# Kernel tuning notes

Measured on AMD Instinct MI355X. Metric: run time of the kernel, lower is better.

## Reference

```python
import jax, jax.numpy as jnp
import numpy as np

N_NODES = 100000
N_EDGES = 50000
NNZ = 800000
D_IN = 128
D_OUT = 128


def setup_inputs() -> dict:
    key = jax.random.key(0)
    k1, k2, k3, k4, k5 = jax.random.split(key, 5)
    x_0 = jax.random.normal(k1, (N_NODES, D_IN), dtype=jnp.float32)
    W = jax.random.normal(k2, (D_OUT, D_IN), dtype=jnp.float32) / np.sqrt(D_IN)
    b = jax.random.normal(k3, (D_OUT,), dtype=jnp.float32) * 0.01
    node_ids = jax.random.randint(k4, (NNZ,), 0, N_NODES, dtype=jnp.int32)
    edge_ids = jax.random.randint(k5, (NNZ,), 0, N_EDGES, dtype=jnp.int32)
    return {"x_0": x_0, "W": W, "b": b, "node_ids": node_ids, "edge_ids": edge_ids}


def reference(x_0, W, b, node_ids, edge_ids):
    # Linear transform (no batchnorm: use_bn=False)
    x = x_0 @ W.T + b  # [n_nodes, out_channels]

    # Step 1: hyperedge aggregation (e_aggr='sum'):  m_{0->1} = B_1^T x, reduce=sum
    m01 = jax.ops.segment_sum(x[node_ids], edge_ids, num_segments=N_EDGES)  # [n_edges, d]

    # Step 2: node aggregation (v_aggr='mean'):  m_{1->0} = B_1 m_{0->1}, reduce=mean
    s = jax.ops.segment_sum(m01[edge_ids], node_ids, num_segments=N_NODES)  # [n_nodes, d]
    cnt = jax.ops.segment_sum(jnp.ones((NNZ,), dtype=x.dtype), node_ids, num_segments=N_NODES)
    m10 = s / jnp.maximum(cnt, 1.0)[:, None]

    # Step 3: SAGE update (residual add)
    return x + m10
```

## Files before the change

kernel.cpp:

```cpp
#include <hip/hip_runtime.h>
#include <hip/hip_bf16.h>

#define NN 100000
#define NE 50000
#define NZ 800000
#define D  128
#define NSEG (NE + NN)
#define FILL_P 4
#define FILL_B 782
#define G_GEMM 782
#define G_HIST 391

typedef __bf16 bf16x8 __attribute__((ext_vector_type(8)));
typedef float f32x4 __attribute__((ext_vector_type(4)));

static __device__ __forceinline__ unsigned short f2bf(float f) {
  union { float f; unsigned u; } v; v.f = f;
  unsigned r = (v.u + 0x7FFFu + ((v.u >> 16) & 1u)) >> 16;
  return (unsigned short)r;
}
static __device__ __forceinline__ float bf2f(unsigned short h) {
  union { unsigned u; float f; } v; v.u = ((unsigned)h) << 16;
  return v.f;
}

__global__ __launch_bounds__(256) void unisage_gemm_hist(const float* __restrict__ x0,
                                                         const float* __restrict__ W,
                                                         const float* __restrict__ bias,
                                                         unsigned short* __restrict__ xb,
                                                         const int* __restrict__ nid,
                                                         const int* __restrict__ eid,
                                                         int* __restrict__ cnt,
                                                         unsigned int* __restrict__ rank) {
  __shared__ __bf16 Wl[128][136];
  if (blockIdx.x < G_GEMM) {
    const int t = threadIdx.x;
#pragma unroll
    for (int i = 0; i < 16; ++i) {
      int idx = i * 1024 + t * 4;
      int dout = idx >> 7;
      int k = idx & 127;
      float4 wv = *(const float4*)(W + idx);
      Wl[dout][k + 0] = (__bf16)wv.x;
      Wl[dout][k + 1] = (__bf16)wv.y;
      Wl[dout][k + 2] = (__bf16)wv.z;
      Wl[dout][k + 3] = (__bf16)wv.w;
    }
    __syncthreads();

    const int wave = t >> 6;
    const int lane = t & 63;
    const int lr = lane & 15;
    const int lg = lane >> 4;
    const int rowbase = blockIdx.x * 128 + wave * 32;

    f32x4 acc[2][8] = {};

#pragma unroll
    for (int ks = 0; ks < 4; ++ks) {
      const int k0 = ks * 32 + lg * 8;
      bf16x8 b[8];
#pragma unroll
      for (int cf = 0; cf < 8; ++cf)
        b[cf] = *(const bf16x8*)&Wl[cf * 16 + lr][k0];
#pragma unroll
      for (int rf = 0; rf < 2; ++rf) {
        int row = rowbase + rf * 16 + lr;
        row = row < NN ? row : NN - 1;
        const float* src = x0 + (size_t)row * D + k0;
        float4 f0 = *(const float4*)(src);
        float4 f1 = *(const float4*)(src + 4);
        bf16x8 a;
        a[0] = (__bf16)f0.x; a[1] = (__bf16)f0.y;
        a[2] = (__bf16)f0.z; a[3] = (__bf16)f0.w;
        a[4] = (__bf16)f1.x; a[5] = (__bf16)f1.y;
        a[6] = (__bf16)f1.z; a[7] = (__bf16)f1.w;
#pragma unroll
        for (int cf = 0; cf < 8; ++cf)
          acc[rf][cf] = __builtin_amdgcn_mfma_f32_16x16x32_bf16(a, b[cf], acc[rf][cf], 0, 0, 0);
      }
    }

#pragma unroll
    for (int cf = 0; cf < 8; ++cf) {
      float bv = bias[cf * 16 + lr];
#pragma unroll
      for (int rf = 0; rf < 2; ++rf) {
#pragma unroll
        for (int r = 0; r < 4; ++r) {
          int row = rowbase + rf * 16 + lg * 4 + r;
          if (row < NN)
            xb[(size_t)row * D + cf * 16 + lr] = f2bf(acc[rf][cf][r] + bv);
        }
      }
    }
  } else {
    int base = ((blockIdx.x - G_GEMM) * 256 + threadIdx.x) * 8;
    if (base >= NZ) return;
    int4 ea = *(const int4*)(eid + base);
    int4 eb = *(const int4*)(eid + base + 4);
    int4 na = *(const int4*)(nid + base);
    int4 nb = *(const int4*)(nid + base + 4);
    int e[8] = {ea.x, ea.y, ea.z, ea.w, eb.x, eb.y, eb.z, eb.w};
    int v[8] = {na.x, na.y, na.z, na.w, nb.x, nb.y, nb.z, nb.w};
    unsigned re[8], rn[8];
#pragma unroll
    for (int j = 0; j < 8; ++j) re[j] = (unsigned)atomicAdd(&cnt[e[j]], 1);
#pragma unroll
    for (int j = 0; j < 8; ++j) rn[j] = (unsigned)atomicAdd(&cnt[NE + v[j]], 1);
    uint4 r0, r1;
    r0.x = (re[0] & 0xffffu) | (rn[0] << 16);
    r0.y = (re[1] & 0xffffu) | (rn[1] << 16);
    r0.z = (re[2] & 0xffffu) | (rn[2] << 16);
    r0.w = (re[3] & 0xffffu) | (rn[3] << 16);
    r1.x = (re[4] & 0xffffu) | (rn[4] << 16);
    r1.y = (re[5] & 0xffffu) | (rn[5] << 16);
    r1.z = (re[6] & 0xffffu) | (rn[6] << 16);
    r1.w = (re[7] & 0xffffu) | (rn[7] << 16);
    *(uint4*)(rank + base) = r0;
    *(uint4*)(rank + base + 4) = r1;
  }
}

__global__ void unisage_scan_k1(const int* __restrict__ in, int* __restrict__ bsum, int n) {
  __shared__ int sh[256];
  int t = threadIdx.x;
  int base = blockIdx.x * 1024 + t * 4;
  int s = 0;
#pragma unroll
  for (int j = 0; j < 4; ++j)
    if (base + j < n) s += in[base + j];
  sh[t] = s;
  __syncthreads();
  for (int o = 128; o > 0; o >>= 1) {
    if (t < o) sh[t] += sh[t + o];
    __syncthreads();
  }
  if (t == 0) bsum[blockIdx.x] = sh[0];
}

__global__ void unisage_scan_k3(const int* __restrict__ in, const int* __restrict__ bsum,
                                int* __restrict__ out, int n, int nb) {
  __shared__ int sh[256];
  int t = threadIdx.x;
  int bv = (t < nb) ? bsum[t] : 0;
  sh[t] = bv;
  __syncthreads();
  for (int o = 1; o < 256; o <<= 1) {
    int add = (t >= o) ? sh[t - o] : 0;
    __syncthreads();
    sh[t] += add;
    __syncthreads();
  }
  int bbase = (blockIdx.x == 0) ? 0 : sh[blockIdx.x - 1];
  __syncthreads();

  int base = blockIdx.x * 1024 + t * 4;
  int v[4];
#pragma unroll
  for (int j = 0; j < 4; ++j) v[j] = (base + j < n) ? in[base + j] : 0;
  int tsum = v[0] + v[1] + v[2] + v[3];
  sh[t] = tsum;
  __syncthreads();
  for (int o = 1; o < 256; o <<= 1) {
    int add = (t >= o) ? sh[t - o] : 0;
    __syncthreads();
    sh[t] += add;
    __syncthreads();
  }
  int run = sh[t] - tsum + bbase;
#pragma unroll
  for (int j = 0; j < 4; ++j) {
    if (base + j < n) out[base + j] = run;
    run += v[j];
  }
}

__global__ void unisage_fill(const int* __restrict__ nid, const int* __restrict__ eid,
                             const unsigned int* __restrict__ rank,
                             const int* __restrict__ off,
                             int* __restrict__ csr_e, int* __restrict__ csr_n) {
  const int R = (NSEG + FILL_P - 1) / FILL_P;
  int pass = blockIdx.x / FILL_B;
  int base = ((blockIdx.x % FILL_B) * 256 + threadIdx.x) * 4;
  if (base >= NZ) return;
  int lo = pass * R, hi = lo + R;
  int4 e4 = *(const int4*)(eid + base);
  int4 n4 = *(const int4*)(nid + base);
  uint4 r4 = *(const uint4*)(rank + base);
  int e[4] = {e4.x, e4.y, e4.z, e4.w};
  int v[4] = {n4.x, n4.y, n4.z, n4.w};
  unsigned r[4] = {r4.x, r4.y, r4.z, r4.w};
#pragma unroll
  for (int j = 0; j < 4; ++j) {
    if (e[j] >= lo && e[j] < hi) csr_e[off[e[j]] + (int)(r[j] & 0xffffu)] = v[j];
    int s = NE + v[j];
    if (s >= lo && s < hi) csr_n[off[s] + (int)(r[j] >> 16) - NZ] = e[j];
  }
}

#define QRED(x) { x += __shfl_xor(x, 16, 64); x += __shfl_xor(x, 32, 64); }

__global__ void unisage_edge_agg(const unsigned short* __restrict__ xb,
                                 const int* __restrict__ csr_e,
                                 const int* __restrict__ off, const int* __restrict__ cnt,
                                 unsigned short* __restrict__ m01b) {
  int w = (blockIdx.x * 256 + threadIdx.x) >> 6;
  int lane = threadIdx.x & 63;
  if (w >= NE) return;
  int quad = lane >> 4;
  int sl = lane & 15;
  int beg = off[w];
  int deg = cnt[w];
  int end = beg + deg;
  float a0 = 0, a1 = 0, a2 = 0, a3 = 0, a4 = 0, a5 = 0, a6 = 0, a7 = 0;
  for (int base = beg; base < end; base += 64) {
    int m = min(64, end - base);
    int idx = (lane < m) ? csr_e[base + lane] : 0;
    int iters = (m + 3) >> 2;
    for (int jj = 0; jj < iters; ++jj) {
      int p = 4 * jj + quad;
      int r = __shfl(idx, p, 64);
      if (p < m) {
        uint4 vv = *(const uint4*)(xb + (size_t)r * D + sl * 8);
        a0 += bf2f((unsigned short)(vv.x & 0xffffu)); a1 += bf2f((unsigned short)(vv.x >> 16));
        a2 += bf2f((unsigned short)(vv.y & 0xffffu)); a3 += bf2f((unsigned short)(vv.y >> 16));
        a4 += bf2f((unsigned short)(vv.z & 0xffffu)); a5 += bf2f((unsigned short)(vv.z >> 16));
        a6 += bf2f((unsigned short)(vv.w & 0xffffu)); a7 += bf2f((unsigned short)(vv.w >> 16));
      }
    }
  }
  QRED(a0) QRED(a1) QRED(a2) QRED(a3) QRED(a4) QRED(a5) QRED(a6) QRED(a7)
  if (quad == 0) {
    uint4 o;
    o.x = (unsigned)f2bf(a0) | ((unsigned)f2bf(a1) << 16);
    o.y = (unsigned)f2bf(a2) | ((unsigned)f2bf(a3) << 16);
    o.z = (unsigned)f2bf(a4) | ((unsigned)f2bf(a5) << 16);
    o.w = (unsigned)f2bf(a6) | ((unsigned)f2bf(a7) << 16);
    *(uint4*)(m01b + (size_t)w * D + sl * 8) = o;
  }
}

__global__ void unisage_node_agg(const unsigned short* __restrict__ xb,
                                 const unsigned short* __restrict__ m01b,
                                 const int* __restrict__ csr_n,
                                 const int* __restrict__ off, const int* __restrict__ cnt,
                                 float* __restrict__ out) {
  int w = (blockIdx.x * 256 + threadIdx.x) >> 6;
  int lane = threadIdx.x & 63;
  if (w >= NN) return;
  int quad = lane >> 4;
  int sl = lane & 15;
  int deg = cnt[NE + w];
  int beg = off[NE + w] - NZ;
  int end = beg + deg;
  float a0 = 0, a1 = 0, a2 = 0, a3 = 0, a4 = 0, a5 = 0, a6 = 0, a7 = 0;
  for (int base = beg; base < end; base += 64) {
    int m = min(64, end - base);
    int idx = (lane < m) ? csr_n[base + lane] : 0;
    int iters = (m + 3) >> 2;
    for (int jj = 0; jj < iters; ++jj) {
      int p = 4 * jj + quad;
      int r = __shfl(idx, p, 64);
      if (p < m) {
        uint4 vv = *(const uint4*)(m01b + (size_t)r * D + sl * 8);
        a0 += bf2f((unsigned short)(vv.x & 0xffffu)); a1 += bf2f((unsigned short)(vv.x >> 16));
        a2 += bf2f((unsigned short)(vv.y & 0xffffu)); a3 += bf2f((unsigned short)(vv.y >> 16));
        a4 += bf2f((unsigned short)(vv.z & 0xffffu)); a5 += bf2f((unsigned short)(vv.z >> 16));
        a6 += bf2f((unsigned short)(vv.w & 0xffffu)); a7 += bf2f((unsigned short)(vv.w >> 16));
      }
    }
  }
  QRED(a0) QRED(a1) QRED(a2) QRED(a3) QRED(a4) QRED(a5) QRED(a6) QRED(a7)
  if (quad == 0) {
    float inv = 1.0f / fmaxf((float)deg, 1.0f);
    uint4 xr = *(const uint4*)(xb + (size_t)w * D + sl * 8);
    float4 o0, o1;
    o0.x = bf2f((unsigned short)(xr.x & 0xffffu)) + a0 * inv;
    o0.y = bf2f((unsigned short)(xr.x >> 16))     + a1 * inv;
    o0.z = bf2f((unsigned short)(xr.y & 0xffffu)) + a2 * inv;
    o0.w = bf2f((unsigned short)(xr.y >> 16))     + a3 * inv;
    o1.x = bf2f((unsigned short)(xr.z & 0xffffu)) + a4 * inv;
    o1.y = bf2f((unsigned short)(xr.z >> 16))     + a5 * inv;
    o1.z = bf2f((unsigned short)(xr.w & 0xffffu)) + a6 * inv;
    o1.w = bf2f((unsigned short)(xr.w >> 16))     + a7 * inv;
    *(float4*)(out + (size_t)w * D + sl * 8) = o0;
    *(float4*)(out + (size_t)w * D + sl * 8 + 4) = o1;
  }
}

extern "C" void kernel_launch(void* const* d_in, const int* in_sizes, int n_in,
                              void* d_out, int out_size, void* d_ws, size_t ws_size,
                              hipStream_t stream) {
  const float* x0   = (const float*)d_in[0];
  const float* W    = (const float*)d_in[1];
  const float* bias = (const float*)d_in[2];
  const int* nid    = (const int*)d_in[3];
  const int* eid    = (const int*)d_in[4];
  float* out = (float*)d_out;

  unsigned short* xb   = (unsigned short*)d_ws;
  unsigned short* m01b = xb + (size_t)NN * D;
  int* cnt   = (int*)(m01b + (size_t)NE * D);
  int* off   = cnt + 150016;
  unsigned int* rank = (unsigned int*)(off + 150016);
  int* csr_e = (int*)(rank + NZ);
  int* csr_n = csr_e + NZ;
  int* bsum  = csr_n + NZ;

  hipMemsetAsync(cnt, 0, NSEG * sizeof(int), stream);

  unisage_gemm_hist<<<G_GEMM + G_HIST, 256, 0, stream>>>(x0, W, bias, xb, nid, eid, cnt, rank);

  const int nb = (NSEG + 1023) / 1024;
  unisage_scan_k1<<<nb, 256, 0, stream>>>(cnt, bsum, NSEG);
  unisage_scan_k3<<<nb, 256, 0, stream>>>(cnt, bsum, off, NSEG, nb);

  unisage_fill<<<FILL_P * FILL_B, 256, 0, stream>>>(nid, eid, rank, off, csr_e, csr_n);

  unisage_edge_agg<<<(NE * 64) / 256, 256, 0, stream>>>(xb, csr_e, off, cnt, m01b);
  unisage_node_agg<<<(NN * 64) / 256, 256, 0, stream>>>(xb, m01b, csr_n, off, cnt, out);
}
```

Measured before the change: 211.1 us.

## Split fused GEMM/histogram kernel, unroll gather loops by two, halve fill passes

The combined GEMM+histogram launch is split back into two separate kernels, giving up the overlap of the atomic histogram with the MFMA GEMM in exchange for simpler per-kernel occupancy. The edge and node gather loops are unrolled by two with predicated (multiply-by-zero) accumulation so two row loads can be in flight at once. The CSR fill pass count is halved from 4 to 2. Together these trade fusion-based overlap for more memory-level parallelism in the gathers and fewer fill passes.

```diff
diff --git a/kernel.cpp b/kernel.cpp
--- a/kernel.cpp
+++ b/kernel.cpp
@@ -6,10 +6,8 @@
 #define NZ 800000
 #define D  128
 #define NSEG (NE + NN)
-#define FILL_P 4
+#define FILL_P 2
 #define FILL_B 782
-#define G_GEMM 782
-#define G_HIST 391
 
 typedef __bf16 bf16x8 __attribute__((ext_vector_type(8)));
 typedef float f32x4 __attribute__((ext_vector_type(4)));
@@ -24,102 +22,99 @@
   return v.f;
 }
 
-__global__ __launch_bounds__(256) void unisage_gemm_hist(const float* __restrict__ x0,
+__global__ __launch_bounds__(256) void unisage_gemm_mfma(const float* __restrict__ x0,
                                                          const float* __restrict__ W,
                                                          const float* __restrict__ bias,
-                                                         unsigned short* __restrict__ xb,
-                                                         const int* __restrict__ nid,
-                                                         const int* __restrict__ eid,
-                                                         int* __restrict__ cnt,
-                                                         unsigned int* __restrict__ rank) {
+                                                         unsigned short* __restrict__ xb) {
   __shared__ __bf16 Wl[128][136];
-  if (blockIdx.x < G_GEMM) {
-    const int t = threadIdx.x;
-#pragma unroll
-    for (int i = 0; i < 16; ++i) {
-      int idx = i * 1024 + t * 4;
-      int dout = idx >> 7;
-      int k = idx & 127;
-      float4 wv = *(const float4*)(W + idx);
-      Wl[dout][k + 0] = (__bf16)wv.x;
-      Wl[dout][k + 1] = (__bf16)wv.y;
-      Wl[dout][k + 2] = (__bf16)wv.z;
-      Wl[dout][k + 3] = (__bf16)wv.w;
-    }
-    __syncthreads();
-
-    const int wave = t >> 6;
-    const int lane = t & 63;
-    const int lr = lane & 15;
-    const int lg = lane >> 4;
-    const int rowbase = blockIdx.x * 128 + wave * 32;
-
-    f32x4 acc[2][8] = {};
-
-#pragma unroll
-    for (int ks = 0; ks < 4; ++ks) {
-      const int k0 = ks * 32 + lg * 8;
-      bf16x8 b[8];
+  const int t = threadIdx.x;
+#pragma unroll
+  for (int i = 0; i < 16; ++i) {
+    int idx = i * 1024 + t * 4;
+    int dout = idx >> 7;
+    int k = idx & 127;
+    float4 wv = *(const float4*)(W + idx);
+    Wl[dout][k + 0] = (__bf16)wv.x;
+    Wl[dout][k + 1] = (__bf16)wv.y;
+    Wl[dout][k + 2] = (__bf16)wv.z;
+    Wl[dout][k + 3] = (__bf16)wv.w;
+  }
+  __syncthreads();
+
+  const int wave = t >> 6;
+  const int lane = t & 63;
+  const int lr = lane & 15;
+  const int lg = lane >> 4;
+  const int rowbase = blockIdx.x * 128 + wave * 32;
+
+  f32x4 acc[2][8] = {};
+
+#pragma unroll
+  for (int ks = 0; ks < 4; ++ks) {
+    const int k0 = ks * 32 + lg * 8;
+    bf16x8 b[8];
+#pragma unroll
+    for (int cf = 0; cf < 8; ++cf)
+      b[cf] = *(const bf16x8*)&Wl[cf * 16 + lr][k0];
+#pragma unroll
+    for (int rf = 0; rf < 2; ++rf) {
+      int row = rowbase + rf * 16 + lr;
+      row = row < NN ? row : NN - 1;
+      const float* src = x0 + (size_t)row * D + k0;
+      float4 f0 = *(const float4*)(src);
+      float4 f1 = *(const float4*)(src + 4);
+      bf16x8 a;
+      a[0] = (__bf16)f0.x; a[1] = (__bf16)f0.y;
+      a[2] = (__bf16)f0.z; a[3] = (__bf16)f0.w;
+      a[4] = (__bf16)f1.x; a[5] = (__bf16)f1.y;
+      a[6] = (__bf16)f1.z; a[7] = (__bf16)f1.w;
 #pragma unroll
       for (int cf = 0; cf < 8; ++cf)
-        b[cf] = *(const bf16x8*)&Wl[cf * 16 + lr][k0];
-#pragma unroll
-      for (int rf = 0; rf < 2; ++rf) {
-        int row = rowbase + rf * 16 + lr;
-        row = row < NN ? row : NN - 1;
-        const float* src = x0 + (size_t)row * D + k0;
-        float4 f0 = *(const float4*)(src);
-        float4 f1 = *(const float4*)(src + 4);
-        bf16x8 a;
-        a[0] = (__bf16)f0.x; a[1] = (__bf16)f0.y;
-        a[2] = (__bf16)f0.z; a[3] = (__bf16)f0.w;
-        a[4] = (__bf16)f1.x; a[5] = (__bf16)f1.y;
-        a[6] = (__bf16)f1.z; a[7] = (__bf16)f1.w;
-#pragma unroll
-        for (int cf = 0; cf < 8; ++cf)
-          acc[rf][cf] = __builtin_amdgcn_mfma_f32_16x16x32_bf16(a, b[cf], acc[rf][cf], 0, 0, 0);
+        acc[rf][cf] = __builtin_amdgcn_mfma_f32_16x16x32_bf16(a, b[cf], acc[rf][cf], 0, 0, 0);
+    }
+  }
+
+#pragma unroll
+  for (int cf = 0; cf < 8; ++cf) {
+    float bv = bias[cf * 16 + lr];
+#pragma unroll
+    for (int rf = 0; rf < 2; ++rf) {
+#pragma unroll
+      for (int r = 0; r < 4; ++r) {
+        int row = rowbase + rf * 16 + lg * 4 + r;
+        if (row < NN)
+          xb[(size_t)row * D + cf * 16 + lr] = f2bf(acc[rf][cf][r] + bv);
       }
     }
-
-#pragma unroll
-    for (int cf = 0; cf < 8; ++cf) {
-      float bv = bias[cf * 16 + lr];
-#pragma unroll
-      for (int rf = 0; rf < 2; ++rf) {
-#pragma unroll
-        for (int r = 0; r < 4; ++r) {
-          int row = rowbase + rf * 16 + lg * 4 + r;
-          if (row < NN)
-            xb[(size_t)row * D + cf * 16 + lr] = f2bf(acc[rf][cf][r] + bv);
-        }
-      }
-    }
-  } else {
-    int base = ((blockIdx.x - G_GEMM) * 256 + threadIdx.x) * 8;
-    if (base >= NZ) return;
-    int4 ea = *(const int4*)(eid + base);
-    int4 eb = *(const int4*)(eid + base + 4);
-    int4 na = *(const int4*)(nid + base);
-    int4 nb = *(const int4*)(nid + base + 4);
-    int e[8] = {ea.x, ea.y, ea.z, ea.w, eb.x, eb.y, eb.z, eb.w};
-    int v[8] = {na.x, na.y, na.z, na.w, nb.x, nb.y, nb.z, nb.w};
-    unsigned re[8], rn[8];
-#pragma unroll
-    for (int j = 0; j < 8; ++j) re[j] = (unsigned)atomicAdd(&cnt[e[j]], 1);
-#pragma unroll
-    for (int j = 0; j < 8; ++j) rn[j] = (unsigned)atomicAdd(&cnt[NE + v[j]], 1);
-    uint4 r0, r1;
-    r0.x = (re[0] & 0xffffu) | (rn[0] << 16);
-    r0.y = (re[1] & 0xffffu) | (rn[1] << 16);
-    r0.z = (re[2] & 0xffffu) | (rn[2] << 16);
-    r0.w = (re[3] & 0xffffu) | (rn[3] << 16);
-    r1.x = (re[4] & 0xffffu) | (rn[4] << 16);
-    r1.y = (re[5] & 0xffffu) | (rn[5] << 16);
-    r1.z = (re[6] & 0xffffu) | (rn[6] << 16);
-    r1.w = (re[7] & 0xffffu) | (rn[7] << 16);
-    *(uint4*)(rank + base) = r0;
-    *(uint4*)(rank + base + 4) = r1;
-  }
+  }
+}
+
+__global__ void unisage_hist_rank(const int* __restrict__ nid, const int* __restrict__ eid,
+                                  int* __restrict__ cnt, unsigned int* __restrict__ rank) {
+  int base = (blockIdx.x * 256 + threadIdx.x) * 8;
+  if (base >= NZ) return;
+  int4 ea = *(const int4*)(eid + base);
+  int4 eb = *(const int4*)(eid + base + 4);
+  int4 na = *(const int4*)(nid + base);
+  int4 nb = *(const int4*)(nid + base + 4);
+  int e[8] = {ea.x, ea.y, ea.z, ea.w, eb.x, eb.y, eb.z, eb.w};
+  int v[8] = {na.x, na.y, na.z, na.w, nb.x, nb.y, nb.z, nb.w};
+  unsigned re[8], rn[8];
+#pragma unroll
+  for (int j = 0; j < 8; ++j) re[j] = (unsigned)atomicAdd(&cnt[e[j]], 1);
+#pragma unroll
+  for (int j = 0; j < 8; ++j) rn[j] = (unsigned)atomicAdd(&cnt[NE + v[j]], 1);
+  uint4 r0, r1;
+  r0.x = (re[0] & 0xffffu) | (rn[0] << 16);
+  r0.y = (re[1] & 0xffffu) | (rn[1] << 16);
+  r0.z = (re[2] & 0xffffu) | (rn[2] << 16);
+  r0.w = (re[3] & 0xffffu) | (rn[3] << 16);
+  r1.x = (re[4] & 0xffffu) | (rn[4] << 16);
+  r1.y = (re[5] & 0xffffu) | (rn[5] << 16);
+  r1.z = (re[6] & 0xffffu) | (rn[6] << 16);
+  r1.w = (re[7] & 0xffffu) | (rn[7] << 16);
+  *(uint4*)(rank + base) = r0;
+  *(uint4*)(rank + base + 4) = r1;
 }
 
 __global__ void unisage_scan_k1(const int* __restrict__ in, int* __restrict__ bsum, int n) {
@@ -201,6 +196,20 @@
 
 #define QRED(x) { x += __shfl_xor(x, 16, 64); x += __shfl_xor(x, 32, 64); }
 
+__device__ __forceinline__ void acc_row(const unsigned short* __restrict__ tab,
+                                        int row, int sl, bool valid, float* a) {
+  uint4 vv = *(const uint4*)(tab + (size_t)row * D + sl * 8);
+  float w = valid ? 1.f : 0.f;
+  a[0] += w * bf2f((unsigned short)(vv.x & 0xffffu));
+  a[1] += w * bf2f((unsigned short)(vv.x >> 16));
+  a[2] += w * bf2f((unsigned short)(vv.y & 0xffffu));
+  a[3] += w * bf2f((unsigned short)(vv.y >> 16));
+  a[4] += w * bf2f((unsigned short)(vv.z & 0xffffu));
+  a[5] += w * bf2f((unsigned short)(vv.z >> 16));
+  a[6] += w * bf2f((unsigned short)(vv.w & 0xffffu));
+  a[7] += w * bf2f((unsigned short)(vv.w >> 16));
+}
+
 __global__ void unisage_edge_agg(const unsigned short* __restrict__ xb,
                                  const int* __restrict__ csr_e,
                                  const int* __restrict__ off, const int* __restrict__ cnt,
@@ -213,30 +222,33 @@
   int beg = off[w];
   int deg = cnt[w];
   int end = beg + deg;
-  float a0 = 0, a1 = 0, a2 = 0, a3 = 0, a4 = 0, a5 = 0, a6 = 0, a7 = 0;
+  float a[8] = {};
   for (int base = beg; base < end; base += 64) {
     int m = min(64, end - base);
     int idx = (lane < m) ? csr_e[base + lane] : 0;
     int iters = (m + 3) >> 2;
-    for (int jj = 0; jj < iters; ++jj) {
-      int p = 4 * jj + quad;
-      int r = __shfl(idx, p, 64);
-      if (p < m) {
-        uint4 vv = *(const uint4*)(xb + (size_t)r * D + sl * 8);
-        a0 += bf2f((unsigned short)(vv.x & 0xffffu)); a1 += bf2f((unsigned short)(vv.x >> 16));
-        a2 += bf2f((unsigned short)(vv.y & 0xffffu)); a3 += bf2f((unsigned short)(vv.y >> 16));
-        a4 += bf2f((unsigned short)(vv.z & 0xffffu)); a5 += bf2f((unsigned short)(vv.z >> 16));
-        a6 += bf2f((unsigned short)(vv.w & 0xffffu)); a7 += bf2f((unsigned short)(vv.w >> 16));
-      }
-    }
-  }
-  QRED(a0) QRED(a1) QRED(a2) QRED(a3) QRED(a4) QRED(a5) QRED(a6) QRED(a7)
+    int jj = 0;
+    for (; jj + 1 < iters; jj += 2) {
+      int p0 = 4 * jj + quad;
+      int p1 = p0 + 4;
+      int r0 = __shfl(idx, p0, 64);
+      int r1 = __shfl(idx, p1, 64);
+      acc_row(xb, r0, sl, p0 < m, a);
+      acc_row(xb, r1, sl, p1 < m, a);
+    }
+    if (jj < iters) {
+      int p0 = 4 * jj + quad;
+      int r0 = __shfl(idx, p0, 64);
+      acc_row(xb, r0, sl, p0 < m, a);
+    }
+  }
+  QRED(a[0]) QRED(a[1]) QRED(a[2]) QRED(a[3]) QRED(a[4]) QRED(a[5]) QRED(a[6]) QRED(a[7])
   if (quad == 0) {
     uint4 o;
-    o.x = (unsigned)f2bf(a0) | ((unsigned)f2bf(a1) << 16);
-    o.y = (unsigned)f2bf(a2) | ((unsigned)f2bf(a3) << 16);
-    o.z = (unsigned)f2bf(a4) | ((unsigned)f2bf(a5) << 16);
-    o.w = (unsigned)f2bf(a6) | ((unsigned)f2bf(a7) << 16);
+    o.x = (unsigned)f2bf(a[0]) | ((unsigned)f2bf(a[1]) << 16);
+    o.y = (unsigned)f2bf(a[2]) | ((unsigned)f2bf(a[3]) << 16);
+    o.z = (unsigned)f2bf(a[4]) | ((unsigned)f2bf(a[5]) << 16);
+    o.w = (unsigned)f2bf(a[6]) | ((unsigned)f2bf(a[7]) << 16);
     *(uint4*)(m01b + (size_t)w * D + sl * 8) = o;
   }
 }
@@ -254,36 +266,39 @@
   int deg = cnt[NE + w];
   int beg = off[NE + w] - NZ;
   int end = beg + deg;
-  float a0 = 0, a1 = 0, a2 = 0, a3 = 0, a4 = 0, a5 = 0, a6 = 0, a7 = 0;
+  float a[8] = {};
   for (int base = beg; base < end; base += 64) {
     int m = min(64, end - base);
     int idx = (lane < m) ? csr_n[base + lane] : 0;
     int iters = (m + 3) >> 2;
-    for (int jj = 0; jj < iters; ++jj) {
-      int p = 4 * jj + quad;
-      int r = __shfl(idx, p, 64);
-      if (p < m) {
-        uint4 vv = *(const uint4*)(m01b + (size_t)r * D + sl * 8);
-        a0 += bf2f((unsigned short)(vv.x & 0xffffu)); a1 += bf2f((unsigned short)(vv.x >> 16));
-        a2 += bf2f((unsigned short)(vv.y & 0xffffu)); a3 += bf2f((unsigned short)(vv.y >> 16));
-        a4 += bf2f((unsigned short)(vv.z & 0xffffu)); a5 += bf2f((unsigned short)(vv.z >> 16));
-        a6 += bf2f((unsigned short)(vv.w & 0xffffu)); a7 += bf2f((unsigned short)(vv.w >> 16));
-      }
-    }
-  }
-  QRED(a0) QRED(a1) QRED(a2) QRED(a3) QRED(a4) QRED(a5) QRED(a6) QRED(a7)
+    int jj = 0;
+    for (; jj + 1 < iters; jj += 2) {
+      int p0 = 4 * jj + quad;
+      int p1 = p0 + 4;
+      int r0 = __shfl(idx, p0, 64);
+      int r1 = __shfl(idx, p1, 64);
+      acc_row(m01b, r0, sl, p0 < m, a);
+      acc_row(m01b, r1, sl, p1 < m, a);
+    }
+    if (jj < iters) {
+      int p0 = 4 * jj + quad;
+      int r0 = __shfl(idx, p0, 64);
+      acc_row(m01b, r0, sl, p0 < m, a);
+    }
+  }
+  QRED(a[0]) QRED(a[1]) QRED(a[2]) QRED(a[3]) QRED(a[4]) QRED(a[5]) QRED(a[6]) QRED(a[7])
   if (quad == 0) {
     float inv = 1.0f / fmaxf((float)deg, 1.0f);
     uint4 xr = *(const uint4*)(xb + (size_t)w * D + sl * 8);
     float4 o0, o1;
-    o0.x = bf2f((unsigned short)(xr.x & 0xffffu)) + a0 * inv;
-    o0.y = bf2f((unsigned short)(xr.x >> 16))     + a1 * inv;
-    o0.z = bf2f((unsigned short)(xr.y & 0xffffu)) + a2 * inv;
-    o0.w = bf2f((unsigned short)(xr.y >> 16))     + a3 * inv;
-    o1.x = bf2f((unsigned short)(xr.z & 0xffffu)) + a4 * inv;
-    o1.y = bf2f((unsigned short)(xr.z >> 16))     + a5 * inv;
-    o1.z = bf2f((unsigned short)(xr.w & 0xffffu)) + a6 * inv;
-    o1.w = bf2f((unsigned short)(xr.w >> 16))     + a7 * inv;
+    o0.x = bf2f((unsigned short)(xr.x & 0xffffu)) + a[0] * inv;
+    o0.y = bf2f((unsigned short)(xr.x >> 16))     + a[1] * inv;
+    o0.z = bf2f((unsigned short)(xr.y & 0xffffu)) + a[2] * inv;
+    o0.w = bf2f((unsigned short)(xr.y >> 16))     + a[3] * inv;
+    o1.x = bf2f((unsigned short)(xr.z & 0xffffu)) + a[4] * inv;
+    o1.y = bf2f((unsigned short)(xr.z >> 16))     + a[5] * inv;
+    o1.z = bf2f((unsigned short)(xr.w & 0xffffu)) + a[6] * inv;
+    o1.w = bf2f((unsigned short)(xr.w >> 16))     + a[7] * inv;
     *(float4*)(out + (size_t)w * D + sl * 8) = o0;
     *(float4*)(out + (size_t)w * D + sl * 8 + 4) = o1;
   }
@@ -310,7 +325,9 @@
 
   hipMemsetAsync(cnt, 0, NSEG * sizeof(int), stream);
 
-  unisage_gemm_hist<<<G_GEMM + G_HIST, 256, 0, stream>>>(x0, W, bias, xb, nid, eid, cnt, rank);
+  unisage_hist_rank<<<(NZ / 8 + 255) / 256, 256, 0, stream>>>(nid, eid, cnt, rank);
+
+  unisage_gemm_mfma<<<(NN + 127) / 128, 256, 0, stream>>>(x0, W, bias, xb);
 
   const int nb = (NSEG + 1023) / 1024;
   unisage_scan_k1<<<nb, 256, 0, stream>>>(cnt, bsum, NSEG);
```

Result: slower. 216.2 us (+2.4%).
